# Performance work log

Measured on AMD Instinct MI355X. Metric: run time of the kernel, lower is better.

The kernel has to match this reference:

```python
import jax, jax.numpy as jnp
import numpy as np

N_AGENTS = 8

def _nearest(x, codebook):
    # x: [N, D], codebook: [K, D] -> indices [N]
    # squared L2 distance via expansion; argmin over codebook axis
    d2 = (jnp.sum(x * x, axis=1, keepdims=True)
          - 2.0 * x @ codebook.T
          + jnp.sum(codebook * codebook, axis=1)[None, :])  # [N, K]
    return jnp.argmin(d2, axis=1)

def setup_inputs() -> dict:
    key = jax.random.key(0)
    ks = jax.random.split(key, 16)
    s = 0.02
    H, D_in, R, K, S = 512, 256, 64, 256, 512
    inp = {
        "inputs": jax.random.normal(ks[0], (131072, D_in), jnp.float32),
        "W0": jax.random.normal(ks[1], (D_in, H), jnp.float32) * s,
        "b0": jnp.zeros((H,), jnp.float32),
        "W1": jax.random.normal(ks[2], (H, H), jnp.float32) * s,
        "b1": jnp.zeros((H,), jnp.float32),
        "W2": jax.random.normal(ks[3], (H, R), jnp.float32) * s,
        "b2": jnp.zeros((R,), jnp.float32),
        "codebook": jax.random.normal(ks[4], (K, R), jnp.float32),
        "W3": jax.random.normal(ks[5], (R, H), jnp.float32) * s,
        "b3": jnp.zeros((H,), jnp.float32),
        "W4": jax.random.normal(ks[6], (N_AGENTS * H, H), jnp.float32) * s,
        "b4": jnp.zeros((H,), jnp.float32),
        "W5": jax.random.normal(ks[7], (H, S), jnp.float32) * s,
        "b5": jnp.zeros((S,), jnp.float32),
    }
    return inp

def reference(inputs, W0, b0, W1, b1, W2, b2, codebook, W3, b3, W4, b4, W5, b5):
    # encode: fc2(relu(fc1(relu(fc0(x)))))
    h = jax.nn.relu(inputs @ W0 + b0)
    h = jax.nn.relu(h @ W1 + b1)
    z_e = h @ W2 + b2  # [N, role_dim]

    # emb(z_e, weight_sg=True): straight-through to z_e, codebook detached
    idx1 = _nearest(z_e, codebook)
    z_q_raw = jnp.take(codebook, idx1, axis=0)
    z_q = z_e + jax.lax.stop_gradient(z_q_raw - z_e)

    # emb(z_e.detach()): grad flows to codebook only (gather -> scatter-add vjp)
    z_e_sg = jax.lax.stop_gradient(z_e)
    idx2 = _nearest(z_e_sg, codebook)
    role_emb = jnp.take(codebook, idx2, axis=0)

    # decode
    rec = jax.nn.relu(z_q @ W3 + b3).reshape(-1, N_AGENTS * W3.shape[1])
    rec = jax.nn.relu(rec @ W4 + b4)
    recon = rec @ W5 + b5  # [N/n_agents, state_dim]
    return recon, z_e, role_emb
```

## Files before the change

### kernel.cpp

```cpp
#include <hip/hip_runtime.h>
#include <hip/hip_bf16.h>
#include <cstddef>

__device__ __forceinline__ unsigned short f2bf(float f) {
    union { float f; unsigned int u; } v; v.f = f;
    unsigned int r = (v.u + 0x7fffu + ((v.u >> 16) & 1u)) >> 16;
    return (unsigned short)r;
}

typedef __bf16    bf16x8 __attribute__((ext_vector_type(8)));
typedef float     f32x4  __attribute__((ext_vector_type(4)));
typedef _Float16  f16x8  __attribute__((ext_vector_type(8)));

#define SPLIT_SCALE 2.44140625e-4f

typedef const __attribute__((address_space(1))) void cglb_t;
typedef __attribute__((address_space(3))) void lds_t;

__device__ __forceinline__ void fsplit(float v, _Float16& hi, _Float16& lo) {
    hi = (_Float16)v;
    lo = (_Float16)((v - (float)hi) * 4096.0f);
}

__device__ __forceinline__ int swz4(int r) { return (r & 3) ^ ((r >> 2) & 3); }

template<int K>
__global__ __launch_bounds__(256, 3)
void gemm_split7(const _Float16* __restrict__ Ahi, const _Float16* __restrict__ Alo,
                 const _Float16* __restrict__ Bhi, const _Float16* __restrict__ Blo,
                 const float* __restrict__ bias,
                 _Float16* __restrict__ Chi, _Float16* __restrict__ Clo,
                 int M, int N)
{
    constexpr int BK = 32;
    constexpr int NS = K / BK;

    __shared__ alignas(16) _Float16 SA[2][2][128 * 32];
    __shared__ alignas(16) _Float16 SB[2][2][64 * 32];

    const int tid  = threadIdx.x;
    const int lane = tid & 63;
    const int w    = tid >> 6;

    int bx = blockIdx.x, by = blockIdx.y;
    {
        const int gx = gridDim.x, nwg = gx * gridDim.y;
        if ((nwg & 7) == 0) {
            int d = bx + by * gx;
            int L = (d & 7) * (nwg >> 3) + (d >> 3);
            bx = L % gx; by = L / gx;
        }
    }
    const int bm = by * 128;
    const int bn = bx * 64;

    f32x4 acc0[2][4], acc1[2][4];
#pragma unroll
    for (int m = 0; m < 2; ++m)
#pragma unroll
        for (int n = 0; n < 4; ++n) {
            acc0[m][n] = (f32x4){0.f, 0.f, 0.f, 0.f};
            acc1[m][n] = (f32x4){0.f, 0.f, 0.f, 0.f};
        }

    auto stage = [&](int buf, int k0) {
#pragma unroll
        for (int pl = 0; pl < 2; ++pl) {
            const _Float16* src = pl ? Alo : Ahi;
#pragma unroll
            for (int j = 0; j < 2; ++j) {
                const int p16 = (w * 2 + j) * 64 + lane;
                const int r   = p16 >> 2;
                const int c   = (p16 & 3) ^ swz4(r);
                const _Float16* g = src + (size_t)(bm + r) * K + k0 + c * 8;
                __builtin_amdgcn_global_load_lds((cglb_t*)g,
                    (lds_t*)&SA[buf][pl][p16 * 8], 16, 0, 0);
            }
            const _Float16* srcB = pl ? Blo : Bhi;
            const int p16b = w * 64 + lane;
            const int rb   = p16b >> 2;
            const int cb   = (p16b & 3) ^ swz4(rb);
            const _Float16* gB = srcB + (size_t)(bn + rb) * K + k0 + cb * 8;
            __builtin_amdgcn_global_load_lds((cglb_t*)gB,
                (lds_t*)&SB[buf][pl][p16b * 8], 16, 0, 0);
        }
    };

    stage(0, 0);
    __syncthreads();

    const int g   = lane >> 4;
    const int r15 = lane & 15;

#pragma unroll
    for (int s = 0; s < NS; ++s) {
        const int p = s & 1;
        if (s + 1 < NS) stage(p ^ 1, (s + 1) * BK);

        f16x8 ah[2], al[2];
#pragma unroll
        for (int m = 0; m < 2; ++m) {
            const int R = w * 32 + m * 16 + r15;
            const int a16 = R * 4 + (g ^ swz4(R));
            ah[m] = *reinterpret_cast<const f16x8*>(&SA[p][0][a16 * 8]);
            al[m] = *reinterpret_cast<const f16x8*>(&SA[p][1][a16 * 8]);
        }
#pragma unroll
        for (int n = 0; n < 4; ++n) {
            const int rB = n * 16 + r15;
            const int b16 = rB * 4 + (g ^ swz4(rB));
            const f16x8 bh = *reinterpret_cast<const f16x8*>(&SB[p][0][b16 * 8]);
            const f16x8 bl = *reinterpret_cast<const f16x8*>(&SB[p][1][b16 * 8]);
#pragma unroll
            for (int m = 0; m < 2; ++m)
                acc0[m][n] = __builtin_amdgcn_mfma_f32_16x16x32_f16(
                    ah[m], bh, acc0[m][n], 0, 0, 0);
#pragma unroll
            for (int m = 0; m < 2; ++m)
                acc1[m][n] = __builtin_amdgcn_mfma_f32_16x16x32_f16(
                    ah[m], bl, acc1[m][n], 0, 0, 0);
#pragma unroll
            for (int m = 0; m < 2; ++m)
                acc1[m][n] = __builtin_amdgcn_mfma_f32_16x16x32_f16(
                    al[m], bh, acc1[m][n], 0, 0, 0);
        }
        __syncthreads();
    }

#pragma unroll
    for (int m = 0; m < 2; ++m)
#pragma unroll
        for (int n = 0; n < 4; ++n) {
            const int col = bn + n * 16 + r15;
            const float bv = bias[col];
#pragma unroll
            for (int q = 0; q < 4; ++q) {
                const int row = bm + w * 32 + m * 16 + (lane >> 4) * 4 + q;
                float v = acc0[m][n][q] + SPLIT_SCALE * acc1[m][n][q] + bv;
                v = fmaxf(v, 0.f);
                _Float16 hi, lo; fsplit(v, hi, lo);
                Chi[(size_t)row * N + col] = hi;
                Clo[(size_t)row * N + col] = lo;
            }
        }
}

template<int K, bool AF32>
__global__ __launch_bounds__(256, AF32 ? 3 : 4)
void gemm_split5(const void* __restrict__ Asrc,
                 const _Float16* __restrict__ Bhi, const _Float16* __restrict__ Blo,
                 const float* __restrict__ bias,
                 _Float16* __restrict__ Chi, _Float16* __restrict__ Clo,
                 int M, int N)
{
    constexpr int BK  = 32;
    constexpr int LDP = 40;
    constexpr int NS  = K / BK;

    __shared__ alignas(16) _Float16 Bh[2][64][LDP];
    __shared__ alignas(16) _Float16 Bl[2][64][LDP];

    const int tid  = threadIdx.x;
    const int lane = tid & 63;
    const int w    = tid >> 6;

    int bx = blockIdx.x, by = blockIdx.y;
    {
        const int gx = gridDim.x, nwg = gx * gridDim.y;
        if ((nwg & 7) == 0) {
            int d = bx + by * gx;
            int L = (d & 7) * (nwg >> 3) + (d >> 3);
            bx = L % gx; by = L / gx;
        }
    }
    const int bm = by * 128;
    const int bn = bx * 64;

    f32x4 acc0[2][4], acc1[2][4];
#pragma unroll
    for (int m = 0; m < 2; ++m)
#pragma unroll
        for (int n = 0; n < 4; ++n) {
            acc0[m][n] = (f32x4){0.f, 0.f, 0.f, 0.f};
            acc1[m][n] = (f32x4){0.f, 0.f, 0.f, 0.f};
        }

    const int arow = bm + w * 32 + (lane & 15);
    const int kgrp = (lane >> 4) * 8;
    const int brow = tid >> 2;
    const int bcol = (tid & 3) * 8;

    const _Float16* Ahi_ = (const _Float16*)Asrc;
    const float*    Af_  = (const float*)Asrc;

    f16x8 ah[2], al[2], ahn[2], aln[2];
    float4 rbh, rbl;

    auto loadB = [&](int k0) {
        const size_t gb = (size_t)(bn + brow) * K + k0 + bcol;
        rbh = *reinterpret_cast<const float4*>(Bhi + gb);
        rbl = *reinterpret_cast<const float4*>(Blo + gb);
    };
    auto storeB = [&](int p) {
        *reinterpret_cast<float4*>(&Bh[p][brow][bcol]) = rbh;
        *reinterpret_cast<float4*>(&Bl[p][brow][bcol]) = rbl;
    };
    auto loadA = [&](int k0, f16x8* h, f16x8* l) {
#pragma unroll
        for (int m = 0; m < 2; ++m) {
            const size_t ga = (size_t)(arow + m * 16) * K + k0 + kgrp;
            if constexpr (AF32) {
                float4 v0 = *reinterpret_cast<const float4*>(Af_ + ga);
                float4 v1 = *reinterpret_cast<const float4*>(Af_ + ga + 4);
                float vv[8] = {v0.x, v0.y, v0.z, v0.w, v1.x, v1.y, v1.z, v1.w};
                f16x8 hh, ll;
#pragma unroll
                for (int j = 0; j < 8; ++j) {
                    _Float16 hi, lo; fsplit(vv[j], hi, lo);
                    hh[j] = hi; ll[j] = lo;
                }
                h[m] = hh; l[m] = ll;
            } else {
                h[m] = *reinterpret_cast<const f16x8*>(Ahi_ + ga);
                l[m] = *reinterpret_cast<const f16x8*>(Ahi_ + (size_t)M * K + ga);
            }
        }
    };

    loadB(0);
    loadA(0, ah, al);
    storeB(0);
    __syncthreads();

#pragma unroll
    for (int s = 0; s < NS; ++s) {
        const int p = s & 1;
        if (s + 1 < NS) {
            loadB((s + 1) * BK);
            loadA((s + 1) * BK, ahn, aln);
        }
#pragma unroll
        for (int n = 0; n < 4; ++n) {
            const f16x8 bh = *reinterpret_cast<const f16x8*>(
                &Bh[p][n * 16 + (lane & 15)][kgrp]);
            const f16x8 bl = *reinterpret_cast<const f16x8*>(
                &Bl[p][n * 16 + (lane & 15)][kgrp]);
#pragma unroll
            for (int m = 0; m < 2; ++m)
                acc0[m][n] = __builtin_amdgcn_mfma_f32_16x16x32_f16(
                    ah[m], bh, acc0[m][n], 0, 0, 0);
#pragma unroll
            for (int m = 0; m < 2; ++m)
                acc1[m][n] = __builtin_amdgcn_mfma_f32_16x16x32_f16(
                    ah[m], bl, acc1[m][n], 0, 0, 0);
#pragma unroll
            for (int m = 0; m < 2; ++m)
                acc1[m][n] = __builtin_amdgcn_mfma_f32_16x16x32_f16(
                    al[m], bh, acc1[m][n], 0, 0, 0);
        }
        if (s + 1 < NS) {
            storeB(p ^ 1);
#pragma unroll
            for (int m = 0; m < 2; ++m) { ah[m] = ahn[m]; al[m] = aln[m]; }
        }
        __syncthreads();
    }

#pragma unroll
    for (int m = 0; m < 2; ++m)
#pragma unroll
        for (int n = 0; n < 4; ++n) {
            const int col = bn + n * 16 + (lane & 15);
            const float bv = bias[col];
#pragma unroll
            for (int q = 0; q < 4; ++q) {
                const int row = bm + w * 32 + m * 16 + (lane >> 4) * 4 + q;
                float v = acc0[m][n][q] + SPLIT_SCALE * acc1[m][n][q] + bv;
                v = fmaxf(v, 0.f);
                _Float16 hi, lo; fsplit(v, hi, lo);
                Chi[(size_t)row * N + col] = hi;
                Clo[(size_t)row * N + col] = lo;
            }
        }
}

__global__ __launch_bounds__(256)
void gemm_ze_mfma(const _Float16* __restrict__ Ahi, const _Float16* __restrict__ Alo,
                  const _Float16* __restrict__ Bhi, const _Float16* __restrict__ Blo,
                  const float* __restrict__ bias, float* __restrict__ C, int M)
{
    constexpr int K = 512, N = 64;
    const int tid  = threadIdx.x;
    const int lane = tid & 63;
    const int w    = tid >> 6;
    const int wr   = (w >> 1) * 64;
    const int wc   = (w & 1) * 32;
    const int bm   = blockIdx.x * 128;

    f32x4 acc0[4][2], acc1[4][2];
#pragma unroll
    for (int m = 0; m < 4; ++m)
#pragma unroll
        for (int n = 0; n < 2; ++n) {
            acc0[m][n] = (f32x4){0.f, 0.f, 0.f, 0.f};
            acc1[m][n] = (f32x4){0.f, 0.f, 0.f, 0.f};
        }

    const int arow = bm + wr + (lane & 15);
    const int kgrp = (lane >> 4) * 8;

#pragma unroll
    for (int ks = 0; ks < K / 32; ++ks) {
        const int k0 = ks * 32 + kgrp;
        f16x8 ah[4], al[4];
#pragma unroll
        for (int m = 0; m < 4; ++m) {
            const size_t ga = (size_t)(arow + m * 16) * K + k0;
            ah[m] = *reinterpret_cast<const f16x8*>(Ahi + ga);
            al[m] = *reinterpret_cast<const f16x8*>(Alo + ga);
        }
#pragma unroll
        for (int n = 0; n < 2; ++n) {
            const size_t gb = (size_t)(wc + n * 16 + (lane & 15)) * K + k0;
            const f16x8 bh = *reinterpret_cast<const f16x8*>(Bhi + gb);
            const f16x8 bl = *reinterpret_cast<const f16x8*>(Blo + gb);
#pragma unroll
            for (int m = 0; m < 4; ++m)
                acc0[m][n] = __builtin_amdgcn_mfma_f32_16x16x32_f16(
                    ah[m], bh, acc0[m][n], 0, 0, 0);
#pragma unroll
            for (int m = 0; m < 4; ++m)
                acc1[m][n] = __builtin_amdgcn_mfma_f32_16x16x32_f16(
                    ah[m], bl, acc1[m][n], 0, 0, 0);
#pragma unroll
            for (int m = 0; m < 4; ++m)
                acc1[m][n] = __builtin_amdgcn_mfma_f32_16x16x32_f16(
                    al[m], bh, acc1[m][n], 0, 0, 0);
        }
    }

#pragma unroll
    for (int m = 0; m < 4; ++m)
#pragma unroll
        for (int n = 0; n < 2; ++n) {
            const int col = wc + n * 16 + (lane & 15);
            const float bv = bias[col];
#pragma unroll
            for (int q = 0; q < 4; ++q) {
                const int row = bm + wr + m * 16 + (lane >> 4) * 4 + q;
                C[(size_t)row * N + col] = acc0[m][n][q] + SPLIT_SCALE * acc1[m][n][q] + bv;
            }
        }
}

#define VQ_EPS 1e-3f
__global__ __launch_bounds__(512)
void vq_mfma(const float* __restrict__ Z, const float* __restrict__ CB,
             const _Float16* __restrict__ Chi, const _Float16* __restrict__ Clo,
             float* __restrict__ OUT, unsigned short* __restrict__ ZQB)
{
    __shared__ float  ccf[256];
    __shared__ double ccd[256];
    __shared__ float  xxf[128];
    __shared__ double xxd[128];
    __shared__ float  redv[4][128];
    __shared__ int    redi[4][128];
    __shared__ float  bv1s[128];
    __shared__ int    bis[128];
    __shared__ int    cand[128][16];
    __shared__ int    ncand[128];
    __shared__ int    fullflag[128];
    __shared__ int    flaglist[128];
    __shared__ int    nflag;

    const int tid  = threadIdx.x;
    const int lane = tid & 63;
    const int w    = tid >> 6;
    const int wr   = (w >> 2) * 64;
    const int wc   = (w & 3) * 64;
    const int bm   = blockIdx.x * 128;

    if (tid == 0) nflag = 0;
    if (tid < 256) {
        const float4* c4 = reinterpret_cast<const float4*>(CB + (size_t)tid * 64);
        double cc = 0.0;
#pragma unroll
        for (int v = 0; v < 16; ++v) {
            float4 f = c4[v];
            cc = fma((double)f.x, (double)f.x, cc);
            cc = fma((double)f.y, (double)f.y, cc);
            cc = fma((double)f.z, (double)f.z, cc);
            cc = fma((double)f.w, (double)f.w, cc);
        }
        ccd[tid] = cc; ccf[tid] = (float)cc;
    }
    if (tid < 128) {
        const float4* z4 = reinterpret_cast<const float4*>(Z + (size_t)(bm + tid) * 64);
        double xx = 0.0;
#pragma unroll
        for (int v = 0; v < 16; ++v) {
            float4 f = z4[v];
            xx = fma((double)f.x, (double)f.x, xx);
            xx = fma((double)f.y, (double)f.y, xx);
            xx = fma((double)f.z, (double)f.z, xx);
            xx = fma((double)f.w, (double)f.w, xx);
        }
        xxd[tid] = xx; xxf[tid] = (float)xx;
        ncand[tid] = 0; fullflag[tid] = 0;
    }
    __syncthreads();

    f32x4 acc0[4][4], acc1[4][4];
#pragma unroll
    for (int m = 0; m < 4; ++m)
#pragma unroll
        for (int n = 0; n < 4; ++n) {
            acc0[m][n] = (f32x4){0.f, 0.f, 0.f, 0.f};
            acc1[m][n] = (f32x4){0.f, 0.f, 0.f, 0.f};
        }

    const int arow = bm + wr + (lane & 15);
    const int kgrp = (lane >> 4) * 8;

#pragma unroll
    for (int ks = 0; ks < 2; ++ks) {
        const int k0 = ks * 32 + kgrp;
        f16x8 ah[4], al[4];
#pragma unroll
        for (int m = 0; m < 4; ++m) {
            const float* src = Z + (size_t)(arow + m * 16) * 64 + k0;
            float4 v0 = *reinterpret_cast<const float4*>(src);
            float4 v1 = *reinterpret_cast<const float4*>(src + 4);
            float vv[8] = {v0.x, v0.y, v0.z, v0.w, v1.x, v1.y, v1.z, v1.w};
            f16x8 hh, ll;
#pragma unroll
            for (int j = 0; j < 8; ++j) {
                _Float16 hi, lo; fsplit(vv[j], hi, lo);
                hh[j] = hi; ll[j] = lo;
            }
            ah[m] = hh; al[m] = ll;
        }
#pragma unroll
        for (int n = 0; n < 4; ++n) {
            const size_t gb = (size_t)(wc + n * 16 + (lane & 15)) * 64 + k0;
            const f16x8 bh = *reinterpret_cast<const f16x8*>(Chi + gb);
            const f16x8 bl = *reinterpret_cast<const f16x8*>(Clo + gb);
#pragma unroll
            for (int m = 0; m < 4; ++m)
                acc0[m][n] = __builtin_amdgcn_mfma_f32_16x16x32_f16(
                    ah[m], bh, acc0[m][n], 0, 0, 0);
#pragma unroll
            for (int m = 0; m < 4; ++m)
                acc1[m][n] = __builtin_amdgcn_mfma_f32_16x16x32_f16(
                    ah[m], bl, acc1[m][n], 0, 0, 0);
#pragma unroll
            for (int m = 0; m < 4; ++m)
                acc1[m][n] = __builtin_amdgcn_mfma_f32_16x16x32_f16(
                    al[m], bh, acc1[m][n], 0, 0, 0);
        }
    }

#pragma unroll
    for (int m = 0; m < 4; ++m)
#pragma unroll
        for (int n = 0; n < 4; ++n) {
            const int col = wc + n * 16 + (lane & 15);
            const float cf = ccf[col];
#pragma unroll
            for (int q = 0; q < 4; ++q) {
                const int rl = wr + m * 16 + (lane >> 4) * 4 + q;
                float dot = acc0[m][n][q] + SPLIT_SCALE * acc1[m][n][q];
                acc0[m][n][q] = (xxf[rl] - 2.0f * dot) + cf;
            }
        }

    float bvr[4][4]; int bir[4][4];
#pragma unroll
    for (int m = 0; m < 4; ++m)
#pragma unroll
        for (int q = 0; q < 4; ++q) {
            float bv = 3.4e38f; int bi = 0;
#pragma unroll
            for (int n = 0; n < 4; ++n) {
                const int col = wc + n * 16 + (lane & 15);
                const float v = acc0[m][n][q];
                if (v < bv || (v == bv && col < bi)) { bv = v; bi = col; }
            }
            bvr[m][q] = bv; bir[m][q] = bi;
        }
#pragma unroll
    for (int mask = 1; mask < 16; mask <<= 1) {
#pragma unroll
        for (int m = 0; m < 4; ++m)
#pragma unroll
            for (int q = 0; q < 4; ++q) {
                float ov = __shfl_xor(bvr[m][q], mask);
                int   oi = __shfl_xor(bir[m][q], mask);
                if (ov < bvr[m][q] || (ov == bvr[m][q] && oi < bir[m][q])) {
                    bvr[m][q] = ov; bir[m][q] = oi;
                }
            }
    }
    if ((lane & 15) == 0) {
#pragma unroll
        for (int m = 0; m < 4; ++m)
#pragma unroll
            for (int q = 0; q < 4; ++q) {
                const int rl = wr + m * 16 + (lane >> 4) * 4 + q;
                redv[w & 3][rl] = bvr[m][q];
                redi[w & 3][rl] = bir[m][q];
            }
    }
    __syncthreads();

    if (tid < 128) {
        float bv = 3.4e38f; int bi = 0;
#pragma unroll
        for (int nw = 0; nw < 4; ++nw) {
            float v = redv[nw][tid];
            if (v < bv) { bv = v; bi = redi[nw][tid]; }
        }
        bv1s[tid] = bv; bis[tid] = bi;
    }
    __syncthreads();

#pragma unroll
    for (int m = 0; m < 4; ++m)
#pragma unroll
        for (int q = 0; q < 4; ++q) {
            const int rl = wr + m * 16 + (lane >> 4) * 4 + q;
            const float thr = bv1s[rl] + VQ_EPS;
#pragma unroll
            for (int n = 0; n < 4; ++n) {
                const int col = wc + n * 16 + (lane & 15);
                if (acc0[m][n][q] <= thr) {
                    int s = atomicAdd(&ncand[rl], 1);
                    if (s < 16) cand[rl][s] = col;
                    else        fullflag[rl] = 1;
                }
            }
        }
    __syncthreads();

    if (tid < 128) {
        const int nc_ = ncand[tid] < 16 ? ncand[tid] : 16;
        if (nc_ > 1 && !fullflag[tid]) {
            const float4* z4p = reinterpret_cast<const float4*>(Z + (size_t)(bm + tid) * 64);
            const double xx = xxd[tid];
            double best = 1.0e300; int bi = 256;
            for (int s = 0; s < nc_; ++s) {
                const int e = cand[tid][s];
                const float4* c4p = reinterpret_cast<const float4*>(CB + (size_t)e * 64);
                double dot = 0.0;
#pragma unroll
                for (int v = 0; v < 16; ++v) {
                    float4 zf = z4p[v], cf4 = c4p[v];
                    dot = fma((double)zf.x, (double)cf4.x, dot);
                    dot = fma((double)zf.y, (double)cf4.y, dot);
                    dot = fma((double)zf.z, (double)cf4.z, dot);
                    dot = fma((double)zf.w, (double)cf4.w, dot);
                }
                double d2x = (xx - 2.0 * dot) + ccd[e];
                if (d2x < best || (d2x == best && e < bi)) { best = d2x; bi = e; }
            }
            bis[tid] = bi;
        }
        if (fullflag[tid]) {
            int s = atomicAdd(&nflag, 1);
            flaglist[s] = tid;
        }
    }
    __syncthreads();

    for (int fi = w; fi < nflag; fi += 8) {
        const int rl = flaglist[fi];
        const float* zr = Z + (size_t)(bm + rl) * 64;
        const double xx = xxd[rl];
        double best = 1.0e300; int bi = 256;
#pragma unroll
        for (int j = 0; j < 4; ++j) {
            const int e = lane + j * 64;
            const float* c = CB + (size_t)e * 64;
            double dot = 0.0;
#pragma unroll
            for (int d = 0; d < 64; ++d)
                dot = fma((double)zr[d], (double)c[d], dot);
            double d2x = (xx - 2.0 * dot) + ccd[e];
            if (d2x < best || (d2x == best && e < bi)) { best = d2x; bi = e; }
        }
#pragma unroll
        for (int mask = 1; mask < 64; mask <<= 1) {
            double ov = __shfl_xor(best, mask);
            int    oi = __shfl_xor(bi, mask);
            if (ov < best || (ov == best && oi < bi)) { best = ov; bi = oi; }
        }
        if (lane == 0) bis[rl] = bi;
    }
    __syncthreads();

    {
        const int row  = tid >> 2;
        const int part = tid & 3;
        const int bi   = bis[row];
        const float4* src = reinterpret_cast<const float4*>(CB + (size_t)bi * 64) + part * 4;
        float* dst = OUT + (size_t)(bm + row) * 64 + part * 16;
        unsigned short* dq = ZQB + (size_t)(bm + row) * 64 + part * 16;
#pragma unroll
        for (int v = 0; v < 4; ++v) {
            float4 f = src[v];
            *reinterpret_cast<float4*>(dst + v * 4) = f;
            ushort4 qb = { f2bf(f.x), f2bf(f.y), f2bf(f.z), f2bf(f.w) };
            *reinterpret_cast<ushort4*>(dq + v * 4) = qb;
        }
    }
}

template<bool RELU, bool OUT_BF16>
__global__ __launch_bounds__(256)
void gemm_mfma_bt(const unsigned short* __restrict__ A,
                  const unsigned short* __restrict__ Bt,
                  const float* __restrict__ bias,
                  void* __restrict__ Cv, int M, int N, int K)
{
    constexpr int BK  = 64;
    constexpr int LDP = BK + 8;

    __shared__ alignas(16) unsigned short Asl[128][LDP];
    __shared__ alignas(16) unsigned short Bsl[128][LDP];

    const int tid  = threadIdx.x;
    const int lane = tid & 63;
    const int w    = tid >> 6;
    const int wr   = (w >> 1) * 64;
    const int wc   = (w & 1) * 64;
    const int bm   = blockIdx.y * 128;
    const int bn   = blockIdx.x * 128;

    f32x4 acc[4][4];
#pragma unroll
    for (int m = 0; m < 4; ++m)
#pragma unroll
        for (int n = 0; n < 4; ++n) acc[m][n] = (f32x4){0.f, 0.f, 0.f, 0.f};

    const int sr = tid >> 1;
    const int sc = (tid & 1) * 32;

    for (int k0 = 0; k0 < K; k0 += BK) {
        {
            const float4* ga = reinterpret_cast<const float4*>(
                &A[(size_t)(bm + sr) * K + k0 + sc]);
            const float4* gb = reinterpret_cast<const float4*>(
                &Bt[(size_t)(bn + sr) * K + k0 + sc]);
            float4 va0 = ga[0], va1 = ga[1], va2 = ga[2], va3 = ga[3];
            float4 vb0 = gb[0], vb1 = gb[1], vb2 = gb[2], vb3 = gb[3];
            float4* da = reinterpret_cast<float4*>(&Asl[sr][sc]);
            float4* db = reinterpret_cast<float4*>(&Bsl[sr][sc]);
            da[0] = va0; da[1] = va1; da[2] = va2; da[3] = va3;
            db[0] = vb0; db[1] = vb1; db[2] = vb2; db[3] = vb3;
        }
        __syncthreads();

#pragma unroll
        for (int ks = 0; ks < 2; ++ks) {
            bf16x8 af[4], bf[4];
            const int kc = ks * 32 + (lane >> 4) * 8;
#pragma unroll
            for (int m = 0; m < 4; ++m)
                af[m] = *reinterpret_cast<const bf16x8*>(
                    &Asl[wr + m * 16 + (lane & 15)][kc]);
#pragma unroll
            for (int n = 0; n < 4; ++n)
                bf[n] = *reinterpret_cast<const bf16x8*>(
                    &Bsl[wc + n * 16 + (lane & 15)][kc]);
#pragma unroll
            for (int m = 0; m < 4; ++m)
#pragma unroll
                for (int n = 0; n < 4; ++n)
                    acc[m][n] = __builtin_amdgcn_mfma_f32_16x16x32_bf16(
                        af[m], bf[n], acc[m][n], 0, 0, 0);
        }
        __syncthreads();
    }

#pragma unroll
    for (int m = 0; m < 4; ++m)
#pragma unroll
        for (int n = 0; n < 4; ++n) {
            const int col = bn + wc + n * 16 + (lane & 15);
            const float bv = bias[col];
#pragma unroll
            for (int q = 0; q < 4; ++q) {
                const int row = bm + wr + m * 16 + (lane >> 4) * 4 + q;
                float v = acc[m][n][q] + bv;
                if (RELU) v = fmaxf(v, 0.f);
                if (OUT_BF16)
                    reinterpret_cast<unsigned short*>(Cv)[(size_t)row * N + col] = f2bf(v);
                else
                    reinterpret_cast<float*>(Cv)[(size_t)row * N + col] = v;
            }
        }
}

__global__ __launch_bounds__(256)
void transpose_bf16(const float* __restrict__ W, unsigned short* __restrict__ Wt,
                    int K, int N)
{
    int idx = blockIdx.x * 256 + threadIdx.x;
    if (idx >= K * N) return;
    int n = idx / K, k = idx % K;
    Wt[idx] = f2bf(W[(size_t)k * N + n]);
}

__global__ __launch_bounds__(256)
void transpose_split_f16(const float* __restrict__ W,
                         _Float16* __restrict__ Whi, _Float16* __restrict__ Wlo,
                         int K, int N)
{
    int idx = blockIdx.x * 256 + threadIdx.x;
    if (idx >= K * N) return;
    int n = idx / K, k = idx % K;
    _Float16 hi, lo; fsplit(W[(size_t)k * N + n], hi, lo);
    Whi[idx] = hi; Wlo[idx] = lo;
}

__global__ __launch_bounds__(256)
void split_flat_f16(const float* __restrict__ src,
                    _Float16* __restrict__ hi, _Float16* __restrict__ lo, int n)
{
    int i = blockIdx.x * 256 + threadIdx.x;
    if (i >= n) return;
    _Float16 h, l; fsplit(src[i], h, l);
    hi[i] = h; lo[i] = l;
}

extern "C" void kernel_launch(void* const* d_in, const int* in_sizes, int n_in,
                              void* d_out, int out_size, void* d_ws, size_t ws_size,
                              hipStream_t stream)
{
    const float* X  = (const float*)d_in[0];
    const float* W0 = (const float*)d_in[1];
    const float* b0 = (const float*)d_in[2];
    const float* W1 = (const float*)d_in[3];
    const float* b1 = (const float*)d_in[4];
    const float* W2 = (const float*)d_in[5];
    const float* b2 = (const float*)d_in[6];
    const float* CB = (const float*)d_in[7];
    const float* W3 = (const float*)d_in[8];
    const float* b3 = (const float*)d_in[9];
    const float* W4 = (const float*)d_in[10];
    const float* b4 = (const float*)d_in[11];
    const float* W5 = (const float*)d_in[12];
    const float* b5 = (const float*)d_in[13];

    const int D_in = 256, H = 512, R = 64, S = 512, NA = 8;
    const int Mtot = in_sizes[0] / D_in;

    float* recon = (float*)d_out;
    float* ze    = recon + (size_t)(Mtot / NA) * S;
    float* remb  = ze + (size_t)Mtot * R;

    char* p = (char*)d_ws;
    _Float16* W0hi = (_Float16*)p;  p += (size_t)H * D_in * 2;
    _Float16* W0lo = (_Float16*)p;  p += (size_t)H * D_in * 2;
    _Float16* W1hi = (_Float16*)p;  p += (size_t)H * H * 2;
    _Float16* W1lo = (_Float16*)p;  p += (size_t)H * H * 2;
    _Float16* W2thi = (_Float16*)p; p += (size_t)R * H * 2;
    _Float16* W2tlo = (_Float16*)p; p += (size_t)R * H * 2;
    _Float16* CBhi = (_Float16*)p;  p += (size_t)256 * R * 2;
    _Float16* CBlo = (_Float16*)p;  p += (size_t)256 * R * 2;
    unsigned short* W3t = (unsigned short*)p;  p += (size_t)H * R * 2;
    unsigned short* W4t = (unsigned short*)p;  p += (size_t)H * (NA * H) * 2;
    unsigned short* W5t = (unsigned short*)p;  p += (size_t)S * H * 2;
    size_t fixed = (size_t)(p - (char*)d_ws);
    fixed = (fixed + 255) & ~(size_t)255;

    int nc = 2;
    while (nc < 128) {
        size_t rpcT = (size_t)Mtot / nc;
        if (fixed + rpcT * 4224 + 1024 <= ws_size) break;
        nc *= 2;
    }
    const int rpc = Mtot / nc;
    char* q = (char*)d_ws + fixed;
    _Float16* h0hi = (_Float16*)q;                 q += (size_t)rpc * H * 2;
    _Float16* h0lo = (_Float16*)q;                 q += (size_t)rpc * H * 2;
    _Float16* h1hi = (_Float16*)q;                 q += (size_t)rpc * H * 2;
    _Float16* h1lo = (_Float16*)q;                 q += (size_t)rpc * H * 2;
    unsigned short* zqb = (unsigned short*)q;      q += (size_t)rpc * R * 2;
    unsigned short* rec1b = (unsigned short*)h0hi;
    unsigned short* rec2b = (unsigned short*)h1hi;

    transpose_split_f16<<<(H * D_in + 255) / 256, 256, 0, stream>>>(W0, W0hi, W0lo, D_in, H);
    transpose_split_f16<<<(H * H + 255) / 256, 256, 0, stream>>>(W1, W1hi, W1lo, H, H);
    transpose_split_f16<<<(H * R + 255) / 256, 256, 0, stream>>>(W2, W2thi, W2tlo, H, R);
    split_flat_f16<<<(256 * R + 255) / 256, 256, 0, stream>>>(CB, CBhi, CBlo, 256 * R);
    transpose_bf16<<<(H * R + 255) / 256, 256, 0, stream>>>(W3, W3t, R, H);
    transpose_bf16<<<(H * NA * H + 255) / 256, 256, 0, stream>>>(W4, W4t, NA * H, H);
    transpose_bf16<<<(S * H + 255) / 256, 256, 0, stream>>>(W5, W5t, H, S);

    for (int r0 = 0; r0 < Mtot; r0 += rpc) {
        const int M6 = rpc / NA;
        gemm_split5<256, true><<<dim3(H / 64, rpc / 128), 256, 0, stream>>>(
            X + (size_t)r0 * D_in, W0hi, W0lo, b0, h0hi, h0lo, rpc, H);
        gemm_split7<512><<<dim3(H / 64, rpc / 128), 256, 0, stream>>>(
            h0hi, h0lo, W1hi, W1lo, b1, h1hi, h1lo, rpc, H);
        gemm_ze_mfma<<<rpc / 128, 256, 0, stream>>>(
            h1hi, h1lo, W2thi, W2tlo, b2, ze + (size_t)r0 * R, rpc);
        vq_mfma<<<rpc / 128, 512, 0, stream>>>(
            ze + (size_t)r0 * R, CB, CBhi, CBlo,
            remb + (size_t)r0 * R, zqb);
        gemm_mfma_bt<true, true><<<dim3(H / 128, rpc / 128), 256, 0, stream>>>(
            zqb, W3t, b3, rec1b, rpc, H, R);
        gemm_mfma_bt<true, true><<<dim3(H / 128, M6 / 128), 256, 0, stream>>>(
            rec1b, W4t, b4, rec2b, M6, H, NA * H);
        gemm_mfma_bt<false, false><<<dim3(S / 128, M6 / 128), 256, 0, stream>>>(
            rec2b, W5t, b5, recon + (size_t)(r0 / NA) * S, M6, S, H);
    }
}
```

Measured before the change: 981.8 us.

## Replace decoder bf16 GEMM with double-buffered direct-to-LDS swizzled kernel

Swaps the decoder GEMM kernel for a new version. The new one streams A and B tiles straight into LDS with global_load_lds, double-buffers them with BK=32 so the next tile loads while the current one computes, and uses an XOR swizzle in place of padding to avoid bank conflicts. It also remaps workgroups in groups of 8 for better L2 locality, and lets the chunk loop start at a single chunk when the workspace is large enough. The risks are more barrier steps per K and the smaller K tile.

```diff
diff --git a/kernel.cpp b/kernel.cpp
--- a/kernel.cpp
+++ b/kernel.cpp
@@ -141,6 +141,109 @@
                 _Float16 hi, lo; fsplit(v, hi, lo);
                 Chi[(size_t)row * N + col] = hi;
                 Clo[(size_t)row * N + col] = lo;
+            }
+        }
+}
+
+template<bool RELU, bool OUT_BF16>
+__global__ __launch_bounds__(256, 3)
+void gemm_bt7(const unsigned short* __restrict__ A,
+              const unsigned short* __restrict__ Bt,
+              const float* __restrict__ bias,
+              void* __restrict__ Cv, int M, int N, int K)
+{
+    constexpr int BK = 32;
+
+    __shared__ alignas(16) unsigned short SA[2][128 * 32];
+    __shared__ alignas(16) unsigned short SB[2][128 * 32];
+
+    const int tid  = threadIdx.x;
+    const int lane = tid & 63;
+    const int w    = tid >> 6;
+    const int wr   = (w >> 1) * 64;
+    const int wc   = (w & 1) * 64;
+
+    int bx = blockIdx.x, by = blockIdx.y;
+    {
+        const int gx = gridDim.x, nwg = gx * gridDim.y;
+        if ((nwg & 7) == 0) {
+            int d = bx + by * gx;
+            int L = (d & 7) * (nwg >> 3) + (d >> 3);
+            bx = L % gx; by = L / gx;
+        }
+    }
+    const int bm = by * 128;
+    const int bn = bx * 128;
+
+    f32x4 acc[4][4];
+#pragma unroll
+    for (int m = 0; m < 4; ++m)
+#pragma unroll
+        for (int n = 0; n < 4; ++n) acc[m][n] = (f32x4){0.f, 0.f, 0.f, 0.f};
+
+    auto stage = [&](int buf, int k0) {
+#pragma unroll
+        for (int j = 0; j < 2; ++j) {
+            const int p16 = (w * 2 + j) * 64 + lane;
+            const int r   = p16 >> 2;
+            const int c   = (p16 & 3) ^ swz4(r);
+            const unsigned short* gA = A + (size_t)(bm + r) * K + k0 + c * 8;
+            __builtin_amdgcn_global_load_lds((cglb_t*)gA,
+                (lds_t*)&SA[buf][p16 * 8], 16, 0, 0);
+            const unsigned short* gB = Bt + (size_t)(bn + r) * K + k0 + c * 8;
+            __builtin_amdgcn_global_load_lds((cglb_t*)gB,
+                (lds_t*)&SB[buf][p16 * 8], 16, 0, 0);
+        }
+    };
+
+    stage(0, 0);
+    __syncthreads();
+
+    const int g   = lane >> 4;
+    const int r15 = lane & 15;
+    const int NS  = K / BK;
+
+    for (int s = 0; s < NS; ++s) {
+        const int p = s & 1;
+        if (s + 1 < NS) stage(p ^ 1, (s + 1) * BK);
+
+        bf16x8 af[4], bf[4];
+#pragma unroll
+        for (int m = 0; m < 4; ++m) {
+            const int R = wr + m * 16 + r15;
+            const int a16 = R * 4 + (g ^ swz4(R));
+            af[m] = *reinterpret_cast<const bf16x8*>(&SA[p][a16 * 8]);
+        }
+#pragma unroll
+        for (int n = 0; n < 4; ++n) {
+            const int RB = wc + n * 16 + r15;
+            const int b16 = RB * 4 + (g ^ swz4(RB));
+            bf[n] = *reinterpret_cast<const bf16x8*>(&SB[p][b16 * 8]);
+        }
+#pragma unroll
+        for (int m = 0; m < 4; ++m)
+#pragma unroll
+            for (int n = 0; n < 4; ++n)
+                acc[m][n] = __builtin_amdgcn_mfma_f32_16x16x32_bf16(
+                    af[m], bf[n], acc[m][n], 0, 0, 0);
+        __syncthreads();
+    }
+
+#pragma unroll
+    for (int m = 0; m < 4; ++m)
+#pragma unroll
+        for (int n = 0; n < 4; ++n) {
+            const int col = bn + wc + n * 16 + r15;
+            const float bv = bias[col];
+#pragma unroll
+            for (int q = 0; q < 4; ++q) {
+                const int row = bm + wr + m * 16 + (lane >> 4) * 4 + q;
+                float v = acc[m][n][q] + bv;
+                if (RELU) v = fmaxf(v, 0.f);
+                if (OUT_BF16)
+                    reinterpret_cast<unsigned short*>(Cv)[(size_t)row * N + col] = f2bf(v);
+                else
+                    reinterpret_cast<float*>(Cv)[(size_t)row * N + col] = v;
             }
         }
 }
@@ -615,92 +718,6 @@
     }
 }
 
-template<bool RELU, bool OUT_BF16>
-__global__ __launch_bounds__(256)
-void gemm_mfma_bt(const unsigned short* __restrict__ A,
-                  const unsigned short* __restrict__ Bt,
-                  const float* __restrict__ bias,
-                  void* __restrict__ Cv, int M, int N, int K)
-{
-    constexpr int BK  = 64;
-    constexpr int LDP = BK + 8;
-
-    __shared__ alignas(16) unsigned short Asl[128][LDP];
-    __shared__ alignas(16) unsigned short Bsl[128][LDP];
-
-    const int tid  = threadIdx.x;
-    const int lane = tid & 63;
-    const int w    = tid >> 6;
-    const int wr   = (w >> 1) * 64;
-    const int wc   = (w & 1) * 64;
-    const int bm   = blockIdx.y * 128;
-    const int bn   = blockIdx.x * 128;
-
-    f32x4 acc[4][4];
-#pragma unroll
-    for (int m = 0; m < 4; ++m)
-#pragma unroll
-        for (int n = 0; n < 4; ++n) acc[m][n] = (f32x4){0.f, 0.f, 0.f, 0.f};
-
-    const int sr = tid >> 1;
-    const int sc = (tid & 1) * 32;
-
-    for (int k0 = 0; k0 < K; k0 += BK) {
-        {
-            const float4* ga = reinterpret_cast<const float4*>(
-                &A[(size_t)(bm + sr) * K + k0 + sc]);
-            const float4* gb = reinterpret_cast<const float4*>(
-                &Bt[(size_t)(bn + sr) * K + k0 + sc]);
-            float4 va0 = ga[0], va1 = ga[1], va2 = ga[2], va3 = ga[3];
-            float4 vb0 = gb[0], vb1 = gb[1], vb2 = gb[2], vb3 = gb[3];
-            float4* da = reinterpret_cast<float4*>(&Asl[sr][sc]);
-            float4* db = reinterpret_cast<float4*>(&Bsl[sr][sc]);
-            da[0] = va0; da[1] = va1; da[2] = va2; da[3] = va3;
-            db[0] = vb0; db[1] = vb1; db[2] = vb2; db[3] = vb3;
-        }
-        __syncthreads();
-
-#pragma unroll
-        for (int ks = 0; ks < 2; ++ks) {
-            bf16x8 af[4], bf[4];
-            const int kc = ks * 32 + (lane >> 4) * 8;
-#pragma unroll
-            for (int m = 0; m < 4; ++m)
-                af[m] = *reinterpret_cast<const bf16x8*>(
-                    &Asl[wr + m * 16 + (lane & 15)][kc]);
-#pragma unroll
-            for (int n = 0; n < 4; ++n)
-                bf[n] = *reinterpret_cast<const bf16x8*>(
-                    &Bsl[wc + n * 16 + (lane & 15)][kc]);
-#pragma unroll
-            for (int m = 0; m < 4; ++m)
-#pragma unroll
-                for (int n = 0; n < 4; ++n)
-                    acc[m][n] = __builtin_amdgcn_mfma_f32_16x16x32_bf16(
-                        af[m], bf[n], acc[m][n], 0, 0, 0);
-        }
-        __syncthreads();
-    }
-
-#pragma unroll
-    for (int m = 0; m < 4; ++m)
-#pragma unroll
-        for (int n = 0; n < 4; ++n) {
-            const int col = bn + wc + n * 16 + (lane & 15);
-            const float bv = bias[col];
-#pragma unroll
-            for (int q = 0; q < 4; ++q) {
-                const int row = bm + wr + m * 16 + (lane >> 4) * 4 + q;
-                float v = acc[m][n][q] + bv;
-                if (RELU) v = fmaxf(v, 0.f);
-                if (OUT_BF16)
-                    reinterpret_cast<unsigned short*>(Cv)[(size_t)row * N + col] = f2bf(v);
-                else
-                    reinterpret_cast<float*>(Cv)[(size_t)row * N + col] = v;
-            }
-        }
-}
-
 __global__ __launch_bounds__(256)
 void transpose_bf16(const float* __restrict__ W, unsigned short* __restrict__ Wt,
                     int K, int N)
@@ -774,7 +791,7 @@
     size_t fixed = (size_t)(p - (char*)d_ws);
     fixed = (fixed + 255) & ~(size_t)255;
 
-    int nc = 2;
+    int nc = 1;
     while (nc < 128) {
         size_t rpcT = (size_t)Mtot / nc;
         if (fixed + rpcT * 4224 + 1024 <= ws_size) break;
@@ -809,11 +826,11 @@
         vq_mfma<<<rpc / 128, 512, 0, stream>>>(
             ze + (size_t)r0 * R, CB, CBhi, CBlo,
             remb + (size_t)r0 * R, zqb);
-        gemm_mfma_bt<true, true><<<dim3(H / 128, rpc / 128), 256, 0, stream>>>(
+        gemm_bt7<true, true><<<dim3(H / 128, rpc / 128), 256, 0, stream>>>(
             zqb, W3t, b3, rec1b, rpc, H, R);
-        gemm_mfma_bt<true, true><<<dim3(H / 128, M6 / 128), 256, 0, stream>>>(
+        gemm_bt7<true, true><<<dim3(H / 128, M6 / 128), 256, 0, stream>>>(
             rec1b, W4t, b4, rec2b, M6, H, NA * H);
-        gemm_mfma_bt<false, false><<<dim3(S / 128, M6 / 128), 256, 0, stream>>>(
+        gemm_bt7<false, false><<<dim3(S / 128, M6 / 128), 256, 0, stream>>>(
             rec2b, W5t, b5, recon + (size_t)(r0 / NA) * S, M6, S, H);
     }
 }
```

Measured after the change: 945.8 us. -3.7%, faster.
